# Performance work log

Measured on AMD Instinct MI355X. Metric: run time of the kernel, lower is better.

## Reference

```python
import jax, jax.numpy as jnp
import numpy as np

RHO = 1.0


def _cayley():
    # Geometric-product structure constants for Cl(2,0), basis (1, e1, e2, e12).
    C = np.zeros((4, 4, 4), dtype=np.float32)
    entries = [
        (0, 0, 0, 1), (0, 1, 1, 1), (0, 2, 2, 1), (0, 3, 3, 1),
        (1, 0, 1, 1), (1, 1, 0, 1), (1, 2, 3, 1), (1, 3, 2, 1),
        (2, 0, 2, 1), (2, 1, 3, -1), (2, 2, 0, 1), (2, 3, 1, -1),
        (3, 0, 3, 1), (3, 1, 2, -1), (3, 2, 1, 1), (3, 3, 0, -1),
    ]
    for x, y, z, s in entries:
        C[x, y, z] = s
    return jnp.asarray(C)

CAYLEY = _cayley()

B, I, O, G, X = 64, 64, 64, 4096, 4
GRID_MIN, GRID_MAX = -2.0, 2.0


def setup_inputs() -> dict:
    key = jax.random.key(0)
    k1, k2, k3 = jax.random.split(key, 3)
    x = jax.random.normal(k1, (B, I, X), dtype=jnp.float32)
    # random_grid: quasirandom points in [grid_min, grid_max]^X (Sobol in torch; uniform here)
    grid = jax.random.uniform(k2, (G, X), dtype=jnp.float32) * (GRID_MAX - GRID_MIN) + GRID_MIN
    weights = jax.random.normal(k3, (I, O, G, X), dtype=jnp.float32)
    silu_weight = jnp.ones((I, O, X), dtype=jnp.float32)
    silu_bias = jnp.zeros((I, O, X), dtype=jnp.float32)
    return {"x": x, "grid": grid, "weights": weights,
            "silu_weight": silu_weight, "silu_bias": silu_bias}


def reference(x, grid, weights, silu_weight, silu_bias):
    # x: (B, I, X); grid: (G, X); weights: (I, O, G, X)
    diff = x[:, :, None, :] - grid[None, None, :, :]          # (B, I, G, X)
    # algebra.norm(v)**2 with Euclidean metric = sum over multivector components
    rbf = jnp.exp(-jnp.sum(diff * diff, axis=-1) / RHO)       # (B, I, G)
    result = jnp.einsum('big,iogx->biox', rbf, weights)       # (B, I, O, X)
    # componentwise SiLU branch: geometric product via cayley tensor
    sx = jax.nn.silu(x)                                       # (B, I, X)
    silu_val = jnp.einsum('iox,biy,xyz->bioz', silu_weight, sx, CAYLEY)
    silu_val = silu_val + silu_bias                           # broadcast (B, I, O, X)
    out = jnp.sum(result + silu_val, axis=1)                  # 'biox->box'
    return out                                                # NoNorm: identity norm
```

## Files before the change

### kernel.cpp

```cpp
#include <hip/hip_runtime.h>
#include <hip/hip_bf16.h>

#define BB 64
#define II 64
#define OO 64
#define GG 4096
#define KP 32
#define NCH 8
#define GC (GG / NCH)
#define NPH (GC / KP)

typedef short bf16x8 __attribute__((ext_vector_type(8)));
typedef short bf16x4 __attribute__((ext_vector_type(4)));
typedef float f32x4  __attribute__((ext_vector_type(4)));

static __device__ __forceinline__ short f2bf(float f) {
    __hip_bfloat16 h = __float2bfloat16(f);
    return __builtin_bit_cast(short, h);
}

static __device__ __forceinline__ void lds_barrier() {
    asm volatile("s_waitcnt lgkmcnt(0)" ::: "memory");
    __builtin_amdgcn_s_barrier();
}

__global__ __launch_bounds__(512, 4)
void kan_main(const float* __restrict__ xg, const float* __restrict__ grd,
              const float* __restrict__ wts, float* __restrict__ dst,
              int atomic_mode)
{
    __shared__ __align__(16) unsigned short Bs[2][256 * KP];
    __shared__ __align__(16) unsigned short As[2][BB * KP];

    const int i  = blockIdx.x;
    const int ch = blockIdx.y;
    const int g0 = ch * GC;

    const int t    = threadIdx.x;
    const int lane = t & 63;
    const int wv   = t >> 6;

    const int c  = t & 31;
    const int r0 = t >> 5;
    const float4* wrow = reinterpret_cast<const float4*>(wts)
                         + (size_t)i * OO * GG + g0 + c;

    const int orow = t >> 3;
    const int gq   = t & 7;
    const float4* gp = reinterpret_cast<const float4*>(grd) + g0 + gq * 4;
    const float4  xv = reinterpret_cast<const float4*>(xg)[orow * II + i];

    f32x4 acc[4][2];
    #pragma unroll
    for (int mt = 0; mt < 4; ++mt)
        #pragma unroll
        for (int nt = 0; nt < 2; ++nt) acc[mt][nt] = {0.f, 0.f, 0.f, 0.f};

    float4 pre[4];
    #pragma unroll
    for (int q = 0; q < 4; ++q)
        pre[q] = wrow[(size_t)(q * 16 + r0) * GG];

    for (int p = 0; p < NPH; ++p) {
        unsigned short* Bb = Bs[p & 1];
        unsigned short* Ab = As[p & 1];

        float4 gv[4];
        #pragma unroll
        for (int q = 0; q < 4; ++q) gv[q] = gp[p * KP + q];

        #pragma unroll
        for (int q = 0; q < 4; ++q) {
            const int   row = q * 16 + r0;
            const float4 w4 = pre[q];
            if (p + 1 < NPH)
                pre[q] = wrow[(size_t)row * GG + (p + 1) * KP];
            unsigned short* bp = &Bb[(row * 4) * KP];
            bp[0 * KP + (c     )] = (unsigned short)f2bf(w4.x);
            bp[1 * KP + (c ^  8)] = (unsigned short)f2bf(w4.y);
            bp[2 * KP + (c ^ 16)] = (unsigned short)f2bf(w4.z);
            bp[3 * KP + (c ^ 24)] = (unsigned short)f2bf(w4.w);
        }

        {
            bf16x4 av;
            #pragma unroll
            for (int q = 0; q < 4; ++q) {
                const float d0 = xv.x - gv[q].x, d1 = xv.y - gv[q].y,
                            d2 = xv.z - gv[q].z, d3 = xv.w - gv[q].w;
                av[q] = f2bf(__expf(-(d0 * d0 + d1 * d1 + d2 * d2 + d3 * d3)));
            }
            *reinterpret_cast<bf16x4*>(
                &Ab[orow * KP + ((gq * 4) ^ ((orow & 3) << 3))]) = av;
        }

        lds_barrier();

        const int lg  = lane >> 4;
        const int r16 = lane & 15;
        bf16x8 af[4], bb[2];
        #pragma unroll
        for (int mt = 0; mt < 4; ++mt) {
            const int r = mt * 16 + r16;
            af[mt] = *reinterpret_cast<const bf16x8*>(
                &As[p & 1][r * KP + ((lg * 8) ^ ((r & 3) << 3))]);
        }
        #pragma unroll
        for (int nt = 0; nt < 2; ++nt) {
            const int r = wv * 32 + nt * 16 + r16;
            bb[nt] = *reinterpret_cast<const bf16x8*>(
                &Bs[p & 1][r * KP + ((lg * 8) ^ ((r & 3) << 3))]);
        }
        #pragma unroll
        for (int mt = 0; mt < 4; ++mt)
            #pragma unroll
            for (int nt = 0; nt < 2; ++nt)
                acc[mt][nt] = __builtin_amdgcn_mfma_f32_16x16x32_bf16(
                    af[mt], bb[nt], acc[mt][nt], 0, 0, 0);
    }

    if (!atomic_mode) {
        float* pp = dst + (size_t)(ch * 64 + i) * (BB * OO * 4);
        #pragma unroll
        for (int mt = 0; mt < 4; ++mt)
            #pragma unroll
            for (int nt = 0; nt < 2; ++nt) {
                const int n  = wv * 32 + nt * 16 + (lane & 15);
                const int mb = mt * 16 + ((lane >> 4) << 2);
                #pragma unroll
                for (int r = 0; r < 4; ++r)
                    pp[(mb + r) * 256 + n] = acc[mt][nt][r];
            }
    } else {
        #pragma unroll
        for (int mt = 0; mt < 4; ++mt)
            #pragma unroll
            for (int nt = 0; nt < 2; ++nt) {
                const int n  = wv * 32 + nt * 16 + (lane & 15);
                const int mb = mt * 16 + ((lane >> 4) << 2);
                #pragma unroll
                for (int r = 0; r < 4; ++r)
                    atomicAdd(&dst[(mb + r) * 256 + n], acc[mt][nt][r]);
            }
    }
}

__global__ void kan_reduce(const float* __restrict__ part,
                           float* __restrict__ part2, int Q)
{
    const int idx = blockIdx.x * 256 + threadIdx.x;
    const int pg  = blockIdx.y;
    const float* p = part + (size_t)pg * Q * 16384 + idx;
    float s = 0.f;
    #pragma unroll 8
    for (int q = 0; q < Q; ++q) s += p[(size_t)q * 16384];
    part2[pg * 16384 + idx] = s;
}

__global__ void kan_out(const float* __restrict__ part2,
                        const float* __restrict__ xg,
                        const float* __restrict__ sw,
                        const float* __restrict__ sb,
                        float* __restrict__ out, int R)
{
    const int t = blockIdx.x * 256 + threadIdx.x;
    const int b = t >> 6, o = t & 63;

    float o0, o1, o2, o3;
    if (R > 0) {
        o0 = o1 = o2 = o3 = 0.f;
        const float4* p2 = reinterpret_cast<const float4*>(part2);
        for (int r = 0; r < R; ++r) {
            const float4 v = p2[(size_t)r * 4096 + t];
            o0 += v.x; o1 += v.y; o2 += v.z; o3 += v.w;
        }
    } else {
        const float4 v = reinterpret_cast<const float4*>(out)[t];
        o0 = v.x; o1 = v.y; o2 = v.z; o3 = v.w;
    }

    const float4* xg4 = reinterpret_cast<const float4*>(xg);
    const float4* sw4 = reinterpret_cast<const float4*>(sw);
    const float4* sb4 = reinterpret_cast<const float4*>(sb);
    #pragma unroll 4
    for (int i = 0; i < II; ++i) {
        const float4 xvv = xg4[b * II + i];
        const float4 swv = sw4[i * OO + o];
        const float4 sbv = sb4[i * OO + o];
        const float s0 = xvv.x / (1.f + __expf(-xvv.x));
        const float s1 = xvv.y / (1.f + __expf(-xvv.y));
        const float s2 = xvv.z / (1.f + __expf(-xvv.z));
        const float s3 = xvv.w / (1.f + __expf(-xvv.w));
        o0 += swv.x * s0 + swv.y * s1 + swv.z * s2 - swv.w * s3 + sbv.x;
        o1 += swv.x * s1 + swv.y * s0 - swv.z * s3 + swv.w * s2 + sbv.y;
        o2 += swv.x * s2 + swv.y * s3 + swv.z * s0 - swv.w * s1 + sbv.z;
        o3 += swv.x * s3 + swv.y * s2 - swv.z * s1 + swv.w * s0 + sbv.w;
    }
    reinterpret_cast<float4*>(out)[t] = make_float4(o0, o1, o2, o3);
}

extern "C" void kernel_launch(void* const* d_in, const int* in_sizes, int n_in,
                              void* d_out, int out_size, void* d_ws, size_t ws_size,
                              hipStream_t stream)
{
    const float* x   = (const float*)d_in[0];
    const float* grd = (const float*)d_in[1];
    const float* w   = (const float*)d_in[2];
    const float* sw  = (const float*)d_in[3];
    const float* sb  = (const float*)d_in[4];
    float* out = (float*)d_out;
    float* ws  = (float*)d_ws;

    const size_t need = ((size_t)64 * NCH + 4) * 16384 * 4;

    if (ws_size >= need) {
        float* part2 = ws + (size_t)64 * NCH * 16384;
        kan_main<<<dim3(64, NCH), 512, 0, stream>>>(x, grd, w, ws, 0);
        kan_reduce<<<dim3(64, 4), 256, 0, stream>>>(ws, part2, 64 * NCH / 4);
        kan_out<<<16, 256, 0, stream>>>(part2, x, sw, sb, out, 4);
    } else {
        hipMemsetAsync(d_out, 0, (size_t)out_size * sizeof(float), stream);
        kan_main<<<dim3(64, NCH), 512, 0, stream>>>(x, grd, w, out, 1);
        kan_out<<<16, 256, 0, stream>>>(nullptr, x, sw, sb, out, 0);
    }
}
```

Before: 85.76 us.

## Double K-tile depth to 64 and remap weight loads to full-wave rows

The K-phase depth grows from 32 to 64 grid points, which halves the number of phases and barriers per block. Each phase now runs two MFMA k-steps. Weight loads are remapped so each wave reads 64 consecutive float4s of one row, giving fully coalesced 1KB rows, and the LDS swizzle is widened to 8-way XOR for the longer rows. The RBF tile is built in two halves per thread. In exchange the kernel uses twice the LDS (64KB with double buffering) and twice the prefetch registers, which can lower occupancy below the launch-bounds target.

```diff
diff --git a/kernel.cpp b/kernel.cpp
--- a/kernel.cpp
+++ b/kernel.cpp
@@ -5,7 +5,7 @@
 #define II 64
 #define OO 64
 #define GG 4096
-#define KP 32
+#define KP 64
 #define NCH 8
 #define GC (GG / NCH)
 #define NPH (GC / KP)
@@ -40,15 +40,16 @@
     const int lane = t & 63;
     const int wv   = t >> 6;
 
-    const int c  = t & 31;
-    const int r0 = t >> 5;
     const float4* wrow = reinterpret_cast<const float4*>(wts)
-                         + (size_t)i * OO * GG + g0 + c;
-
-    const int orow = t >> 3;
-    const int gq   = t & 7;
-    const float4* gp = reinterpret_cast<const float4*>(grd) + g0 + gq * 4;
-    const float4  xv = reinterpret_cast<const float4*>(xg)[orow * II + i];
+                         + (size_t)i * OO * GG + g0 + lane;
+
+    const int brow = t >> 3;
+    const int oct  = t & 7;
+    const float4* gp = reinterpret_cast<const float4*>(grd) + g0 + oct * 8;
+    const float4  xv = reinterpret_cast<const float4*>(xg)[brow * II + i];
+
+    const int lg  = lane >> 4;
+    const int r16 = lane & 15;
 
     f32x4 acc[4][2];
     #pragma unroll
@@ -56,67 +57,72 @@
         #pragma unroll
         for (int nt = 0; nt < 2; ++nt) acc[mt][nt] = {0.f, 0.f, 0.f, 0.f};
 
-    float4 pre[4];
+    float4 pre[8];
     #pragma unroll
-    for (int q = 0; q < 4; ++q)
-        pre[q] = wrow[(size_t)(q * 16 + r0) * GG];
+    for (int q = 0; q < 8; ++q)
+        pre[q] = wrow[(size_t)(q * 8 + wv) * GG];
 
     for (int p = 0; p < NPH; ++p) {
         unsigned short* Bb = Bs[p & 1];
         unsigned short* Ab = As[p & 1];
 
-        float4 gv[4];
-        #pragma unroll
-        for (int q = 0; q < 4; ++q) gv[q] = gp[p * KP + q];
-
-        #pragma unroll
-        for (int q = 0; q < 4; ++q) {
-            const int   row = q * 16 + r0;
+        #pragma unroll
+        for (int q = 0; q < 8; ++q) {
+            const int   row = q * 8 + wv;
             const float4 w4 = pre[q];
             if (p + 1 < NPH)
                 pre[q] = wrow[(size_t)row * GG + (p + 1) * KP];
-            unsigned short* bp = &Bb[(row * 4) * KP];
-            bp[0 * KP + (c     )] = (unsigned short)f2bf(w4.x);
-            bp[1 * KP + (c ^  8)] = (unsigned short)f2bf(w4.y);
-            bp[2 * KP + (c ^ 16)] = (unsigned short)f2bf(w4.z);
-            bp[3 * KP + (c ^ 24)] = (unsigned short)f2bf(w4.w);
-        }
-
-        {
+            const float wf[4] = {w4.x, w4.y, w4.z, w4.w};
+            #pragma unroll
+            for (int x = 0; x < 4; ++x) {
+                const int n = row * 4 + x;
+                Bb[n * KP + (lane ^ ((n & 7) << 3))] =
+                    (unsigned short)f2bf(wf[x]);
+            }
+        }
+
+        #pragma unroll
+        for (int h = 0; h < 2; ++h) {
+            float4 gv[4];
+            #pragma unroll
+            for (int e = 0; e < 4; ++e) gv[e] = gp[p * KP + h * 4 + e];
             bf16x4 av;
             #pragma unroll
-            for (int q = 0; q < 4; ++q) {
-                const float d0 = xv.x - gv[q].x, d1 = xv.y - gv[q].y,
-                            d2 = xv.z - gv[q].z, d3 = xv.w - gv[q].w;
-                av[q] = f2bf(__expf(-(d0 * d0 + d1 * d1 + d2 * d2 + d3 * d3)));
-            }
+            for (int e = 0; e < 4; ++e) {
+                const float d0 = xv.x - gv[e].x, d1 = xv.y - gv[e].y,
+                            d2 = xv.z - gv[e].z, d3 = xv.w - gv[e].w;
+                av[e] = f2bf(__expf(-(d0*d0 + d1*d1 + d2*d2 + d3*d3)));
+            }
+            const int kb = oct * 8 + h * 4;
             *reinterpret_cast<bf16x4*>(
-                &Ab[orow * KP + ((gq * 4) ^ ((orow & 3) << 3))]) = av;
+                &Ab[brow * KP + (kb ^ ((brow & 7) << 3))]) = av;
         }
 
         lds_barrier();
 
-        const int lg  = lane >> 4;
-        const int r16 = lane & 15;
-        bf16x8 af[4], bb[2];
-        #pragma unroll
-        for (int mt = 0; mt < 4; ++mt) {
-            const int r = mt * 16 + r16;
-            af[mt] = *reinterpret_cast<const bf16x8*>(
-                &As[p & 1][r * KP + ((lg * 8) ^ ((r & 3) << 3))]);
-        }
-        #pragma unroll
-        for (int nt = 0; nt < 2; ++nt) {
-            const int r = wv * 32 + nt * 16 + r16;
-            bb[nt] = *reinterpret_cast<const bf16x8*>(
-                &Bs[p & 1][r * KP + ((lg * 8) ^ ((r & 3) << 3))]);
-        }
-        #pragma unroll
-        for (int mt = 0; mt < 4; ++mt)
-            #pragma unroll
-            for (int nt = 0; nt < 2; ++nt)
-                acc[mt][nt] = __builtin_amdgcn_mfma_f32_16x16x32_bf16(
-                    af[mt], bb[nt], acc[mt][nt], 0, 0, 0);
+        #pragma unroll
+        for (int kk = 0; kk < 2; ++kk) {
+            const int kb = kk * 32 + lg * 8;
+            bf16x8 af[4], bb[2];
+            #pragma unroll
+            for (int mt = 0; mt < 4; ++mt) {
+                const int r = mt * 16 + r16;
+                af[mt] = *reinterpret_cast<const bf16x8*>(
+                    &Ab[r * KP + (kb ^ ((r & 7) << 3))]);
+            }
+            #pragma unroll
+            for (int nt = 0; nt < 2; ++nt) {
+                const int r = wv * 32 + nt * 16 + r16;
+                bb[nt] = *reinterpret_cast<const bf16x8*>(
+                    &Bb[r * KP + (kb ^ ((r & 7) << 3))]);
+            }
+            #pragma unroll
+            for (int mt = 0; mt < 4; ++mt)
+                #pragma unroll
+                for (int nt = 0; nt < 2; ++nt)
+                    acc[mt][nt] = __builtin_amdgcn_mfma_f32_16x16x32_bf16(
+                        af[mt], bb[nt], acc[mt][nt], 0, 0, 0);
+        }
     }
 
     if (!atomic_mode) {
```

Measured after the change: 159.7 us. 1.86x slower.
